# Kernel optimization log

Hardware: AMD Instinct MI355X
Metric: run time of the kernel (lower is better)

The kernel has to match this reference:

```python
import jax, jax.numpy as jnp
import numpy as np

N_NODES = 100000
N_EDGES = 1600000
IN_DIM = 64
OUT_DIM = 64


def setup_inputs() -> dict:
    key = jax.random.key(0)
    k_x, k_e, k_wm, k_bm, k_wu, k_bu = jax.random.split(key, 6)
    x = jax.random.normal(k_x, (N_NODES, IN_DIM), dtype=jnp.float32)
    edge_index = jax.random.randint(k_e, (2, N_EDGES), 0, N_NODES, dtype=jnp.int64)
    # PyTorch Linear default init: U(-1/sqrt(fan_in), 1/sqrt(fan_in))
    lim_m = 1.0 / np.sqrt(2 * IN_DIM)
    lim_u = 1.0 / np.sqrt(IN_DIM + OUT_DIM)
    W_msg = jax.random.uniform(k_wm, (2 * IN_DIM, OUT_DIM), jnp.float32, -lim_m, lim_m)
    b_msg = jax.random.uniform(k_bm, (OUT_DIM,), jnp.float32, -lim_m, lim_m)
    W_upd = jax.random.uniform(k_wu, (IN_DIM + OUT_DIM, OUT_DIM), jnp.float32, -lim_u, lim_u)
    b_upd = jax.random.uniform(k_bu, (OUT_DIM,), jnp.float32, -lim_u, lim_u)
    return {"x": x, "edge_index": edge_index, "W_msg": W_msg, "b_msg": b_msg,
            "W_upd": W_upd, "b_upd": b_upd}


def reference(x, edge_index, W_msg, b_msg, W_upd, b_upd):
    num_nodes = x.shape[0]
    source, target = edge_index[0], edge_index[1]
    # gather endpoint features and compute messages: [E, 2*in] -> [E, out]
    edge_feats = jnp.concatenate([x[source], x[target]], axis=-1)
    messages = jax.nn.relu(edge_feats @ W_msg + b_msg)
    # mean aggregation onto target nodes
    agg_sum = jax.ops.segment_sum(messages, target, num_segments=num_nodes)
    counts = jax.ops.segment_sum(jnp.ones_like(target, dtype=x.dtype), target,
                                 num_segments=num_nodes)
    aggregated = agg_sum / jnp.clip(counts, 1.0, None)[:, None]
    # update MLP: [N, in+out] -> [N, out]
    updated = jax.nn.relu(jnp.concatenate([x, aggregated], axis=-1) @ W_upd + b_upd)
    return updated
```

## Files before the change

kernel.cpp:

```cpp
#include <hip/hip_runtime.h>
#include <hip/hip_bf16.h>

#define N_NODES 100000
#define N_EDGES 1600000
#define DIM 64
#define NB 196
#define CAP 9216
#define SMASK 0x1FFFFu
#define PBLOCKS 391
#define TBLOCKS 1563

typedef __attribute__((ext_vector_type(8))) short bf16x8;
typedef __attribute__((ext_vector_type(4))) float f32x4;
typedef __attribute__((ext_vector_type(2))) float f32x2;

__device__ __forceinline__ unsigned short f2bs(float f) {
    __hip_bfloat16 h = __float2bfloat16(f);
    return *reinterpret_cast<unsigned short*>(&h);
}

__global__ __launch_bounds__(256) void transform_partition(
    const float* __restrict__ x, const float* __restrict__ W_msg,
    const float* __restrict__ b_msg,
    unsigned int* __restrict__ Xs8, unsigned int* __restrict__ Xt8,
    const int* __restrict__ eidx, int* __restrict__ bcursor,
    unsigned int* __restrict__ pairs,
    const float* __restrict__ W_upd, unsigned short* __restrict__ wfrag)
{
    __shared__ __align__(16) char smem[35200];
    const int tid = threadIdx.x, lane = tid & 63, wid = tid >> 6;

    if (blockIdx.x >= PBLOCKS + TBLOCKS) {
        for (int i = tid; i < 8192; i += 256) {
            const int j = i & 7, l = (i >> 3) & 63, kk = (i >> 9) & 3, ct = i >> 11;
            const int hi = l >> 4;
            int k;
            if (kk < 2) k = kk * 32 + (hi << 3) + j;
            else        k = 64 + ((j & 3) << 4) + ((kk - 2) << 3) + (hi << 1) + (j >> 2);
            const int c = ct * 16 + (l & 15);
            wfrag[i] = f2bs(W_upd[k * 64 + c]);
        }
    } else if (blockIdx.x >= PBLOCKS) {
        unsigned short* WB = reinterpret_cast<unsigned short*>(smem);
        const int tb = blockIdx.x - PBLOCKS;

        for (int i = tid; i < 8192; i += 256) {
            const int j = i & 7, l = (i >> 3) & 63, kk = (i >> 9) & 1, ct = i >> 10;
            const int k = kk * 32 + ((l >> 4) << 3) + j;
            const int c = ct * 16 + (l & 15);
            WB[i] = f2bs(W_msg[(((c >> 6) << 6) + k) * 64 + (c & 63)]);
        }
        __syncthreads();

        const int r0 = tb * 64 + wid * 16;
        if (r0 >= N_NODES) return;

        f32x4 acc[8];
        #pragma unroll
        for (int ct = 0; ct < 8; ++ct) acc[ct] = (f32x4){0.f, 0.f, 0.f, 0.f};

        const int r = r0 + (lane & 15);
        #pragma unroll
        for (int kk = 0; kk < 2; ++kk) {
            const int off = kk * 32 + ((lane >> 4) << 3);
            const float4* xp = reinterpret_cast<const float4*>(&x[r * 64 + off]);
            const float4 p0 = xp[0], p1 = xp[1];
            bf16x8 a;
            a[0] = (short)f2bs(p0.x); a[1] = (short)f2bs(p0.y);
            a[2] = (short)f2bs(p0.z); a[3] = (short)f2bs(p0.w);
            a[4] = (short)f2bs(p1.x); a[5] = (short)f2bs(p1.y);
            a[6] = (short)f2bs(p1.z); a[7] = (short)f2bs(p1.w);
            #pragma unroll
            for (int ct = 0; ct < 8; ++ct) {
                const bf16x8 b = *reinterpret_cast<const bf16x8*>(
                    &WB[(((ct << 1) | kk) * 64 + lane) << 3]);
                acc[ct] = __builtin_amdgcn_mfma_f32_16x16x32_bf16(a, b, acc[ct], 0, 0, 0);
            }
        }

        const int fr = lane & 15;
        const int rb = r0 + ((lane >> 4) << 2);
        const float bj0 = b_msg[fr],      bj1 = b_msg[16 + fr];
        const float bj2 = b_msg[32 + fr], bj3 = b_msg[48 + fr];
        #pragma unroll
        for (int q = 0; q < 4; ++q) {
            unsigned int xs = 0;
            xs = (unsigned)__builtin_amdgcn_cvt_pk_fp8_f32(acc[0][q], acc[1][q], (int)xs, false);
            xs = (unsigned)__builtin_amdgcn_cvt_pk_fp8_f32(acc[2][q], acc[3][q], (int)xs, true);
            Xs8[(rb + q) * 16 + fr] = xs;
            unsigned int xt = 0;
            xt = (unsigned)__builtin_amdgcn_cvt_pk_fp8_f32(acc[4][q] + bj0, acc[5][q] + bj1, (int)xt, false);
            xt = (unsigned)__builtin_amdgcn_cvt_pk_fp8_f32(acc[6][q] + bj2, acc[7][q] + bj3, (int)xt, true);
            Xt8[(rb + q) * 16 + fr] = xt;
        }
    } else {
        unsigned int* sbuf = reinterpret_cast<unsigned int*>(smem);
        int* dbase = reinterpret_cast<int*>(smem + 16384);
        int* tcnt  = reinterpret_cast<int*>(smem + 32768);
        int* toff  = tcnt + NB;
        int* gpos  = toff + NB;
        int* wsum  = gpos + NB;

        const int base = blockIdx.x * 4096;
        const int tcount = min(4096, N_EDGES - base);
        if (tid < NB) tcnt[tid] = 0;
        __syncthreads();

        unsigned int pk[16]; int bb[16]; int rk[16];
        #pragma unroll
        for (int j = 0; j < 16; ++j) {
            const int idx = base + j * 256 + tid;
            bb[j] = -1;
            if (idx < N_EDGES) {
                const int sv = eidx[idx];
                const int tv = eidx[N_EDGES + idx];
                bb[j] = tv >> 9;
                pk[j] = (unsigned)sv | ((unsigned)(tv & 511) << 17);
                rk[j] = atomicAdd(&tcnt[bb[j]], 1);
            }
        }
        __syncthreads();

        const int v = (tid < NB) ? tcnt[tid] : 0;
        int s = v;
        #pragma unroll
        for (int d = 1; d < 64; d <<= 1) { int u = __shfl_up(s, d); if (lane >= d) s += u; }
        if (lane == 63) wsum[wid] = s;
        __syncthreads();
        if (wid == 0) {
            int ws = (lane < 4) ? wsum[lane] : 0;
            #pragma unroll
            for (int d = 1; d < 4; d <<= 1) { int u = __shfl_up(ws, d); if (lane >= d) ws += u; }
            if (lane < 4) wsum[lane] = ws;
        }
        __syncthreads();
        const int exc = (wid ? wsum[wid - 1] : 0) + s - v;
        if (tid < NB) {
            toff[tid] = exc;
            gpos[tid] = tid * CAP + (v ? atomicAdd(&bcursor[tid], v) : 0);
        }
        __syncthreads();

        #pragma unroll
        for (int j = 0; j < 16; ++j) {
            if (bb[j] >= 0) {
                const int l = toff[bb[j]] + rk[j];
                sbuf[l]  = pk[j];
                dbase[l] = gpos[bb[j]] + rk[j];
            }
        }
        __syncthreads();
        for (int i = tid; i < tcount; i += 256)
            pairs[dbase[i]] = sbuf[i];
    }
}

__global__ __launch_bounds__(1024) void bucket_sort(const int* __restrict__ bcursor,
                                                    const unsigned int* __restrict__ pairs,
                                                    int* __restrict__ csr,
                                                    int* __restrict__ deg,
                                                    int* __restrict__ row)
{
    __shared__ unsigned int ebuf[CAP];
    __shared__ unsigned short rbuf[CAP];
    __shared__ int ncnt[512], noff[512];
    __shared__ int wsum[8];
    const int tid = threadIdx.x, lane = tid & 63, wid = tid >> 6;
    const int b = blockIdx.x;
    const int s0 = b * CAP;
    const int cnt = bcursor[b];
    if (tid < 512) ncnt[tid] = 0;
    __syncthreads();

    for (int i = tid; i < cnt; i += 1024) {
        const unsigned int p = pairs[s0 + i];
        ebuf[i] = p;
        rbuf[i] = (unsigned short)atomicAdd(&ncnt[p >> 17], 1);
    }
    __syncthreads();

    int v = 0, s = 0;
    if (tid < 512) {
        v = ncnt[tid];
        s = v;
        #pragma unroll
        for (int d = 1; d < 64; d <<= 1) { int u = __shfl_up(s, d); if (lane >= d) s += u; }
        if (lane == 63) wsum[wid] = s;
    }
    __syncthreads();
    if (wid == 0) {
        int ws = (lane < 8) ? wsum[lane] : 0;
        #pragma unroll
        for (int d = 1; d < 8; d <<= 1) { int u = __shfl_up(ws, d); if (lane >= d) ws += u; }
        if (lane < 8) wsum[lane] = ws;
    }
    __syncthreads();
    if (tid < 512) {
        const int exc = (wid ? wsum[wid - 1] : 0) + s - v;
        noff[tid] = exc;
        const int n = b * 512 + tid;
        if (n < N_NODES) { deg[n] = v; row[n] = s0 + exc; }
    }
    __syncthreads();

    for (int i = tid; i < cnt; i += 1024) {
        const unsigned int p = ebuf[i];
        csr[s0 + noff[p >> 17] + (int)rbuf[i]] = (int)(p & SMASK);
    }
}

__device__ __forceinline__ void acc_fp8(unsigned int u,
    float t0, float t1, float t2, float t3,
    float& a0, float& a1, float& a2, float& a3)
{
    const f32x2 lo = __builtin_amdgcn_cvt_pk_f32_fp8(u, false);
    const f32x2 hi = __builtin_amdgcn_cvt_pk_f32_fp8(u, true);
    a0 += fmaxf(lo.x + t0, 0.f);
    a1 += fmaxf(lo.y + t1, 0.f);
    a2 += fmaxf(hi.x + t2, 0.f);
    a3 += fmaxf(hi.y + t3, 0.f);
}

__global__ __launch_bounds__(1024, 8) void agg_update(
    const int* __restrict__ row, const int* __restrict__ deg,
    const int* __restrict__ csr,
    const unsigned int* __restrict__ Xs8, const unsigned int* __restrict__ Xt8,
    const float* __restrict__ x, const unsigned short* __restrict__ wfrag,
    const float* __restrict__ b_upd, float* __restrict__ out)
{
    __shared__ unsigned short WB[8192];
    __shared__ uint2 aggT[16][18];

    const int tid = threadIdx.x, lane = tid & 63, w = tid >> 6;
    const int n0 = blockIdx.x * 16;

    reinterpret_cast<bf16x8*>(WB)[tid] = reinterpret_cast<const bf16x8*>(wfrag)[tid];

    const int n = n0 + w;
    const int c = lane & 15, q = lane >> 4;
    const int start = row[n], d = deg[n];
    const unsigned int tp = Xt8[n * 16 + c];
    const f32x2 tlo = __builtin_amdgcn_cvt_pk_f32_fp8(tp, false);
    const f32x2 thi = __builtin_amdgcn_cvt_pk_f32_fp8(tp, true);
    const float t0 = tlo.x, t1 = tlo.y, t2 = thi.x, t3 = thi.y;
    float a0 = 0.f, a1 = 0.f, a2 = 0.f, a3 = 0.f;

    if (d > 0) {
        int i = 0;
        for (; i + 32 <= d; i += 32) {
            int sv[8];
            #pragma unroll
            for (int k = 0; k < 8; ++k) sv[k] = csr[start + i + 4 * k + q];
            unsigned int u[8];
            #pragma unroll
            for (int k = 0; k < 8; ++k) u[k] = Xs8[sv[k] * 16 + c];
            #pragma unroll
            for (int k = 0; k < 8; ++k) acc_fp8(u[k], t0, t1, t2, t3, a0, a1, a2, a3);
        }
        const int rem = d - i;
        if (rem > 0) {
            const int lastIdx = start + d - 1;
            int sv[8]; bool vm[8];
            #pragma unroll
            for (int k = 0; k < 8; ++k) {
                const int e = i + 4 * k + q;
                vm[k] = (e < d);
                sv[k] = csr[vm[k] ? (start + e) : lastIdx];
            }
            unsigned int u[8];
            #pragma unroll
            for (int k = 0; k < 8; ++k) u[k] = Xs8[sv[k] * 16 + c];
            #pragma unroll
            for (int k = 0; k < 8; ++k) {
                const f32x2 lo = __builtin_amdgcn_cvt_pk_f32_fp8(u[k], false);
                const f32x2 hi = __builtin_amdgcn_cvt_pk_f32_fp8(u[k], true);
                if (vm[k]) {
                    a0 += fmaxf(lo.x + t0, 0.f);
                    a1 += fmaxf(lo.y + t1, 0.f);
                    a2 += fmaxf(hi.x + t2, 0.f);
                    a3 += fmaxf(hi.y + t3, 0.f);
                }
            }
        }
    }

    a0 += __shfl_xor(a0, 16); a0 += __shfl_xor(a0, 32);
    a1 += __shfl_xor(a1, 16); a1 += __shfl_xor(a1, 32);
    a2 += __shfl_xor(a2, 16); a2 += __shfl_xor(a2, 32);
    a3 += __shfl_xor(a3, 16); a3 += __shfl_xor(a3, 32);
    if (q == 0) {
        const float inv = (d > 0) ? 1.0f / (float)d : 0.f;
        uint2 v2;
        v2.x = (unsigned)f2bs(a0 * inv) | ((unsigned)f2bs(a1 * inv) << 16);
        v2.y = (unsigned)f2bs(a2 * inv) | ((unsigned)f2bs(a3 * inv) << 16);
        aggT[w][c] = v2;
    }
    __syncthreads();

    if (w < 4) {
        const int ct = w;
        f32x4 acc = (f32x4){0.f, 0.f, 0.f, 0.f};
        const int fr = lane & 15, hi = lane >> 4;
        const int r = n0 + fr;
        #pragma unroll
        for (int kk = 0; kk < 4; ++kk) {
            bf16x8 a;
            if (kk < 2) {
                const float4* xp = reinterpret_cast<const float4*>(
                    &x[r * 64 + kk * 32 + (hi << 3)]);
                const float4 p0 = xp[0], p1 = xp[1];
                a[0] = (short)f2bs(p0.x); a[1] = (short)f2bs(p0.y);
                a[2] = (short)f2bs(p0.z); a[3] = (short)f2bs(p0.w);
                a[4] = (short)f2bs(p1.x); a[5] = (short)f2bs(p1.y);
                a[6] = (short)f2bs(p1.z); a[7] = (short)f2bs(p1.w);
            } else {
                a = *reinterpret_cast<const bf16x8*>(
                    &aggT[fr][((kk - 2) << 3) + (hi << 1)]);
            }
            const bf16x8 b = *reinterpret_cast<const bf16x8*>(
                &WB[(((ct << 2) | kk) * 64 + lane) << 3]);
            acc = __builtin_amdgcn_mfma_f32_16x16x32_bf16(a, b, acc, 0, 0, 0);
        }
        const int rb = n0 + (hi << 2);
        const int cc = ct * 16 + fr;
        const float bj = b_upd[cc];
        #pragma unroll
        for (int qq = 0; qq < 4; ++qq)
            out[(rb + qq) * 64 + cc] = fmaxf(acc[qq] + bj, 0.f);
    }
}

extern "C" void kernel_launch(void* const* d_in, const int* in_sizes, int n_in,
                              void* d_out, int out_size, void* d_ws, size_t ws_size,
                              hipStream_t stream) {
    const float* x     = (const float*)d_in[0];
    const int*   eidx  = (const int*)  d_in[1];
    const float* W_msg = (const float*)d_in[2];
    const float* b_msg = (const float*)d_in[3];
    const float* W_upd = (const float*)d_in[4];
    const float* b_upd = (const float*)d_in[5];
    float* out = (float*)d_out;

    int* deg     = (int*)d_ws;
    int* row     = deg + N_NODES;
    int* bcursor = row + N_NODES;
    unsigned short* wfrag = (unsigned short*)(bcursor + 256);
    unsigned int* pairs = (unsigned int*)(wfrag + 8192);
    int* csr     = (int*)(pairs + NB * CAP);
    unsigned int* Xs8 = (unsigned int*)(csr + NB * CAP);
    unsigned int* Xt8 = Xs8 + (size_t)N_NODES * 16;

    hipMemsetAsync(bcursor, 0, NB * sizeof(int), stream);
    transform_partition<<<PBLOCKS + TBLOCKS + 1, 256, 0, stream>>>(
        x, W_msg, b_msg, Xs8, Xt8, eidx, bcursor, pairs, W_upd, wfrag);
    bucket_sort<<<NB, 1024, 0, stream>>>(bcursor, pairs, csr, deg, row);
    agg_update<<<N_NODES / 16, 1024, 0, stream>>>(row, deg, csr, Xs8, Xt8,
                                                  x, wfrag, b_upd, out);
}
```

Baseline: 105.4 us.

## Split node transform across partition and sort kernels to balance load

Half of the per-node message transform (first 781 tiles) stays in the partition kernel; the remaining rows move into the bucket-sort kernel as extra 1024-thread blocks running alongside the 196 sort blocks. The aim is to fill idle CUs during the sort kernel, which previously had only 196 blocks. In the aggregation/update kernel, the x row loads and the bias load are hoisted to the kernel start so their latency overlaps the gather phase. Each transform block in the sort kernel rebuilds the W_msg fragment in shared memory, and the hoisted loads keep extra registers live through the gather phase.

```diff
diff --git a/kernel.cpp b/kernel.cpp
--- a/kernel.cpp
+++ b/kernel.cpp
@@ -7,8 +7,10 @@
 #define NB 196
 #define CAP 9216
 #define SMASK 0x1FFFFu
-#define PBLOCKS 391
-#define TBLOCKS 1563
+#define P1 391
+#define T1 781
+#define R1 (T1 * 64)
+#define T2 196
 
 typedef __attribute__((ext_vector_type(8))) short bf16x8;
 typedef __attribute__((ext_vector_type(4))) float f32x4;
@@ -19,7 +21,53 @@
     return *reinterpret_cast<unsigned short*>(&h);
 }
 
-__global__ __launch_bounds__(256) void transform_partition(
+__device__ __forceinline__ void transform_tile(
+    const float* __restrict__ x, const unsigned short* WB,
+    const float* __restrict__ b_msg,
+    unsigned int* __restrict__ Xs8, unsigned int* __restrict__ Xt8,
+    int r0, int lane)
+{
+    f32x4 acc[8];
+    #pragma unroll
+    for (int ct = 0; ct < 8; ++ct) acc[ct] = (f32x4){0.f, 0.f, 0.f, 0.f};
+
+    const int r = r0 + (lane & 15);
+    #pragma unroll
+    for (int kk = 0; kk < 2; ++kk) {
+        const int off = kk * 32 + ((lane >> 4) << 3);
+        const float4* xp = reinterpret_cast<const float4*>(&x[r * 64 + off]);
+        const float4 p0 = xp[0], p1 = xp[1];
+        bf16x8 a;
+        a[0] = (short)f2bs(p0.x); a[1] = (short)f2bs(p0.y);
+        a[2] = (short)f2bs(p0.z); a[3] = (short)f2bs(p0.w);
+        a[4] = (short)f2bs(p1.x); a[5] = (short)f2bs(p1.y);
+        a[6] = (short)f2bs(p1.z); a[7] = (short)f2bs(p1.w);
+        #pragma unroll
+        for (int ct = 0; ct < 8; ++ct) {
+            const bf16x8 b = *reinterpret_cast<const bf16x8*>(
+                &WB[(((ct << 1) | kk) * 64 + lane) << 3]);
+            acc[ct] = __builtin_amdgcn_mfma_f32_16x16x32_bf16(a, b, acc[ct], 0, 0, 0);
+        }
+    }
+
+    const int fr = lane & 15;
+    const int rb = r0 + ((lane >> 4) << 2);
+    const float bj0 = b_msg[fr],      bj1 = b_msg[16 + fr];
+    const float bj2 = b_msg[32 + fr], bj3 = b_msg[48 + fr];
+    #pragma unroll
+    for (int q = 0; q < 4; ++q) {
+        unsigned int xs = 0;
+        xs = (unsigned)__builtin_amdgcn_cvt_pk_fp8_f32(acc[0][q], acc[1][q], (int)xs, false);
+        xs = (unsigned)__builtin_amdgcn_cvt_pk_fp8_f32(acc[2][q], acc[3][q], (int)xs, true);
+        Xs8[(rb + q) * 16 + fr] = xs;
+        unsigned int xt = 0;
+        xt = (unsigned)__builtin_amdgcn_cvt_pk_fp8_f32(acc[4][q] + bj0, acc[5][q] + bj1, (int)xt, false);
+        xt = (unsigned)__builtin_amdgcn_cvt_pk_fp8_f32(acc[6][q] + bj2, acc[7][q] + bj3, (int)xt, true);
+        Xt8[(rb + q) * 16 + fr] = xt;
+    }
+}
+
+__global__ __launch_bounds__(256) void k1_part_xform(
     const float* __restrict__ x, const float* __restrict__ W_msg,
     const float* __restrict__ b_msg,
     unsigned int* __restrict__ Xs8, unsigned int* __restrict__ Xt8,
@@ -30,7 +78,7 @@
     __shared__ __align__(16) char smem[35200];
     const int tid = threadIdx.x, lane = tid & 63, wid = tid >> 6;
 
-    if (blockIdx.x >= PBLOCKS + TBLOCKS) {
+    if (blockIdx.x >= P1 + T1) {
         for (int i = tid; i < 8192; i += 256) {
             const int j = i & 7, l = (i >> 3) & 63, kk = (i >> 9) & 3, ct = i >> 11;
             const int hi = l >> 4;
@@ -40,10 +88,9 @@
             const int c = ct * 16 + (l & 15);
             wfrag[i] = f2bs(W_upd[k * 64 + c]);
         }
-    } else if (blockIdx.x >= PBLOCKS) {
+    } else if (blockIdx.x >= P1) {
         unsigned short* WB = reinterpret_cast<unsigned short*>(smem);
-        const int tb = blockIdx.x - PBLOCKS;
-
+        const int tb = blockIdx.x - P1;
         for (int i = tid; i < 8192; i += 256) {
             const int j = i & 7, l = (i >> 3) & 63, kk = (i >> 9) & 1, ct = i >> 10;
             const int k = kk * 32 + ((l >> 4) << 3) + j;
@@ -51,48 +98,7 @@
             WB[i] = f2bs(W_msg[(((c >> 6) << 6) + k) * 64 + (c & 63)]);
         }
         __syncthreads();
-
-        const int r0 = tb * 64 + wid * 16;
-        if (r0 >= N_NODES) return;
-
-        f32x4 acc[8];
-        #pragma unroll
-        for (int ct = 0; ct < 8; ++ct) acc[ct] = (f32x4){0.f, 0.f, 0.f, 0.f};
-
-        const int r = r0 + (lane & 15);
-        #pragma unroll
-        for (int kk = 0; kk < 2; ++kk) {
-            const int off = kk * 32 + ((lane >> 4) << 3);
-            const float4* xp = reinterpret_cast<const float4*>(&x[r * 64 + off]);
-            const float4 p0 = xp[0], p1 = xp[1];
-            bf16x8 a;
-            a[0] = (short)f2bs(p0.x); a[1] = (short)f2bs(p0.y);
-            a[2] = (short)f2bs(p0.z); a[3] = (short)f2bs(p0.w);
-            a[4] = (short)f2bs(p1.x); a[5] = (short)f2bs(p1.y);
-            a[6] = (short)f2bs(p1.z); a[7] = (short)f2bs(p1.w);
-            #pragma unroll
-            for (int ct = 0; ct < 8; ++ct) {
-                const bf16x8 b = *reinterpret_cast<const bf16x8*>(
-                    &WB[(((ct << 1) | kk) * 64 + lane) << 3]);
-                acc[ct] = __builtin_amdgcn_mfma_f32_16x16x32_bf16(a, b, acc[ct], 0, 0, 0);
-            }
-        }
-
-        const int fr = lane & 15;
-        const int rb = r0 + ((lane >> 4) << 2);
-        const float bj0 = b_msg[fr],      bj1 = b_msg[16 + fr];
-        const float bj2 = b_msg[32 + fr], bj3 = b_msg[48 + fr];
-        #pragma unroll
-        for (int q = 0; q < 4; ++q) {
-            unsigned int xs = 0;
-            xs = (unsigned)__builtin_amdgcn_cvt_pk_fp8_f32(acc[0][q], acc[1][q], (int)xs, false);
-            xs = (unsigned)__builtin_amdgcn_cvt_pk_fp8_f32(acc[2][q], acc[3][q], (int)xs, true);
-            Xs8[(rb + q) * 16 + fr] = xs;
-            unsigned int xt = 0;
-            xt = (unsigned)__builtin_amdgcn_cvt_pk_fp8_f32(acc[4][q] + bj0, acc[5][q] + bj1, (int)xt, false);
-            xt = (unsigned)__builtin_amdgcn_cvt_pk_fp8_f32(acc[6][q] + bj2, acc[7][q] + bj3, (int)xt, true);
-            Xt8[(rb + q) * 16 + fr] = xt;
-        }
+        transform_tile(x, WB, b_msg, Xs8, Xt8, tb * 64 + wid * 16, lane);
     } else {
         unsigned int* sbuf = reinterpret_cast<unsigned int*>(smem);
         int* dbase = reinterpret_cast<int*>(smem + 16384);
@@ -155,57 +161,77 @@
     }
 }
 
-__global__ __launch_bounds__(1024) void bucket_sort(const int* __restrict__ bcursor,
-                                                    const unsigned int* __restrict__ pairs,
-                                                    int* __restrict__ csr,
-                                                    int* __restrict__ deg,
-                                                    int* __restrict__ row)
-{
-    __shared__ unsigned int ebuf[CAP];
-    __shared__ unsigned short rbuf[CAP];
-    __shared__ int ncnt[512], noff[512];
-    __shared__ int wsum[8];
+__global__ __launch_bounds__(1024) void k2_sort_xform(
+    const int* __restrict__ bcursor, const unsigned int* __restrict__ pairs,
+    int* __restrict__ csr, int* __restrict__ deg, int* __restrict__ row,
+    const float* __restrict__ x, const float* __restrict__ W_msg,
+    const float* __restrict__ b_msg,
+    unsigned int* __restrict__ Xs8, unsigned int* __restrict__ Xt8)
+{
+    __shared__ __align__(16) char smem[59424];
     const int tid = threadIdx.x, lane = tid & 63, wid = tid >> 6;
-    const int b = blockIdx.x;
-    const int s0 = b * CAP;
-    const int cnt = bcursor[b];
-    if (tid < 512) ncnt[tid] = 0;
-    __syncthreads();
-
-    for (int i = tid; i < cnt; i += 1024) {
-        const unsigned int p = pairs[s0 + i];
-        ebuf[i] = p;
-        rbuf[i] = (unsigned short)atomicAdd(&ncnt[p >> 17], 1);
-    }
-    __syncthreads();
-
-    int v = 0, s = 0;
-    if (tid < 512) {
-        v = ncnt[tid];
-        s = v;
-        #pragma unroll
-        for (int d = 1; d < 64; d <<= 1) { int u = __shfl_up(s, d); if (lane >= d) s += u; }
-        if (lane == 63) wsum[wid] = s;
-    }
-    __syncthreads();
-    if (wid == 0) {
-        int ws = (lane < 8) ? wsum[lane] : 0;
-        #pragma unroll
-        for (int d = 1; d < 8; d <<= 1) { int u = __shfl_up(ws, d); if (lane >= d) ws += u; }
-        if (lane < 8) wsum[lane] = ws;
-    }
-    __syncthreads();
-    if (tid < 512) {
-        const int exc = (wid ? wsum[wid - 1] : 0) + s - v;
-        noff[tid] = exc;
-        const int n = b * 512 + tid;
-        if (n < N_NODES) { deg[n] = v; row[n] = s0 + exc; }
-    }
-    __syncthreads();
-
-    for (int i = tid; i < cnt; i += 1024) {
-        const unsigned int p = ebuf[i];
-        csr[s0 + noff[p >> 17] + (int)rbuf[i]] = (int)(p & SMASK);
+
+    if (blockIdx.x >= NB) {
+        unsigned short* WB = reinterpret_cast<unsigned short*>(smem);
+        const int tb = blockIdx.x - NB;
+        for (int i = tid; i < 8192; i += 1024) {
+            const int j = i & 7, l = (i >> 3) & 63, kk = (i >> 9) & 1, ct = i >> 10;
+            const int k = kk * 32 + ((l >> 4) << 3) + j;
+            const int c = ct * 16 + (l & 15);
+            WB[i] = f2bs(W_msg[(((c >> 6) << 6) + k) * 64 + (c & 63)]);
+        }
+        __syncthreads();
+        const int r0 = R1 + tb * 256 + wid * 16;
+        if (r0 >= N_NODES) return;
+        transform_tile(x, WB, b_msg, Xs8, Xt8, r0, lane);
+    } else {
+        unsigned int*   ebuf = reinterpret_cast<unsigned int*>(smem);
+        unsigned short* rbuf = reinterpret_cast<unsigned short*>(smem + 36864);
+        int* ncnt = reinterpret_cast<int*>(smem + 55296);
+        int* noff = reinterpret_cast<int*>(smem + 57344);
+        int* wsum = reinterpret_cast<int*>(smem + 59392);
+
+        const int b = blockIdx.x;
+        const int s0 = b * CAP;
+        const int cnt = bcursor[b];
+        if (tid < 512) ncnt[tid] = 0;
+        __syncthreads();
+
+        for (int i = tid; i < cnt; i += 1024) {
+            const unsigned int p = pairs[s0 + i];
+            ebuf[i] = p;
+            rbuf[i] = (unsigned short)atomicAdd(&ncnt[p >> 17], 1);
+        }
+        __syncthreads();
+
+        int v = 0, s = 0;
+        if (tid < 512) {
+            v = ncnt[tid];
+            s = v;
+            #pragma unroll
+            for (int d = 1; d < 64; d <<= 1) { int u = __shfl_up(s, d); if (lane >= d) s += u; }
+            if (lane == 63) wsum[wid] = s;
+        }
+        __syncthreads();
+        if (wid == 0) {
+            int ws = (lane < 8) ? wsum[lane] : 0;
+            #pragma unroll
+            for (int d = 1; d < 8; d <<= 1) { int u = __shfl_up(ws, d); if (lane >= d) ws += u; }
+            if (lane < 8) wsum[lane] = ws;
+        }
+        __syncthreads();
+        if (tid < 512) {
+            const int exc = (wid ? wsum[wid - 1] : 0) + s - v;
+            noff[tid] = exc;
+            const int n = b * 512 + tid;
+            if (n < N_NODES) { deg[n] = v; row[n] = s0 + exc; }
+        }
+        __syncthreads();
+
+        for (int i = tid; i < cnt; i += 1024) {
+            const unsigned int p = ebuf[i];
+            csr[s0 + noff[p >> 17] + (int)rbuf[i]] = (int)(p & SMASK);
+        }
     }
 }
 
@@ -233,6 +259,17 @@
 
     const int tid = threadIdx.x, lane = tid & 63, w = tid >> 6;
     const int n0 = blockIdx.x * 16;
+    const int fr = lane & 15, hi = lane >> 4;
+
+    float4 px0, px1, px2, px3; float bj = 0.f;
+    if (w < 4) {
+        const int r = n0 + fr;
+        const float4* xp = reinterpret_cast<const float4*>(&x[r * 64 + (hi << 3)]);
+        px0 = xp[0]; px1 = xp[1];
+        const float4* xq = reinterpret_cast<const float4*>(&x[r * 64 + 32 + (hi << 3)]);
+        px2 = xq[0]; px3 = xq[1];
+        bj = b_upd[w * 16 + fr];
+    }
 
     reinterpret_cast<bf16x8*>(WB)[tid] = reinterpret_cast<const bf16x8*>(wfrag)[tid];
 
@@ -273,12 +310,12 @@
             #pragma unroll
             for (int k = 0; k < 8; ++k) {
                 const f32x2 lo = __builtin_amdgcn_cvt_pk_f32_fp8(u[k], false);
-                const f32x2 hi = __builtin_amdgcn_cvt_pk_f32_fp8(u[k], true);
+                const f32x2 hi2 = __builtin_amdgcn_cvt_pk_f32_fp8(u[k], true);
                 if (vm[k]) {
                     a0 += fmaxf(lo.x + t0, 0.f);
                     a1 += fmaxf(lo.y + t1, 0.f);
-                    a2 += fmaxf(hi.x + t2, 0.f);
-                    a3 += fmaxf(hi.y + t3, 0.f);
+                    a2 += fmaxf(hi2.x + t2, 0.f);
+                    a3 += fmaxf(hi2.y + t3, 0.f);
                 }
             }
         }
@@ -300,19 +337,19 @@
     if (w < 4) {
         const int ct = w;
         f32x4 acc = (f32x4){0.f, 0.f, 0.f, 0.f};
-        const int fr = lane & 15, hi = lane >> 4;
-        const int r = n0 + fr;
         #pragma unroll
         for (int kk = 0; kk < 4; ++kk) {
             bf16x8 a;
-            if (kk < 2) {
-                const float4* xp = reinterpret_cast<const float4*>(
-                    &x[r * 64 + kk * 32 + (hi << 3)]);
-                const float4 p0 = xp[0], p1 = xp[1];
-                a[0] = (short)f2bs(p0.x); a[1] = (short)f2bs(p0.y);
-                a[2] = (short)f2bs(p0.z); a[3] = (short)f2bs(p0.w);
-                a[4] = (short)f2bs(p1.x); a[5] = (short)f2bs(p1.y);
-                a[6] = (short)f2bs(p1.z); a[7] = (short)f2bs(p1.w);
+            if (kk == 0) {
+                a[0] = (short)f2bs(px0.x); a[1] = (short)f2bs(px0.y);
+                a[2] = (short)f2bs(px0.z); a[3] = (short)f2bs(px0.w);
+                a[4] = (short)f2bs(px1.x); a[5] = (short)f2bs(px1.y);
+                a[6] = (short)f2bs(px1.z); a[7] = (short)f2bs(px1.w);
+            } else if (kk == 1) {
+                a[0] = (short)f2bs(px2.x); a[1] = (short)f2bs(px2.y);
+                a[2] = (short)f2bs(px2.z); a[3] = (short)f2bs(px2.w);
+                a[4] = (short)f2bs(px3.x); a[5] = (short)f2bs(px3.y);
+                a[6] = (short)f2bs(px3.z); a[7] = (short)f2bs(px3.w);
             } else {
                 a = *reinterpret_cast<const bf16x8*>(
                     &aggT[fr][((kk - 2) << 3) + (hi << 1)]);
@@ -323,7 +360,6 @@
         }
         const int rb = n0 + (hi << 2);
         const int cc = ct * 16 + fr;
-        const float bj = b_upd[cc];
         #pragma unroll
         for (int qq = 0; qq < 4; ++qq)
             out[(rb + qq) * 64 + cc] = fmaxf(acc[qq] + bj, 0.f);
@@ -351,9 +387,10 @@
     unsigned int* Xt8 = Xs8 + (size_t)N_NODES * 16;
 
     hipMemsetAsync(bcursor, 0, NB * sizeof(int), stream);
-    transform_partition<<<PBLOCKS + TBLOCKS + 1, 256, 0, stream>>>(
+    k1_part_xform<<<P1 + T1 + 1, 256, 0, stream>>>(
         x, W_msg, b_msg, Xs8, Xt8, eidx, bcursor, pairs, W_upd, wfrag);
-    bucket_sort<<<NB, 1024, 0, stream>>>(bcursor, pairs, csr, deg, row);
+    k2_sort_xform<<<NB + T2, 1024, 0, stream>>>(
+        bcursor, pairs, csr, deg, row, x, W_msg, b_msg, Xs8, Xt8);
     agg_update<<<N_NODES / 16, 1024, 0, stream>>>(row, deg, csr, Xs8, Xt8,
                                                   x, wfrag, b_upd, out);
 }
```

Result: faster. 102.1 us, median of 2 (-3.1%).
